# Kernel tuning notes

Hardware: AMD Instinct MI355X
Metric: run time of the kernel (lower is better)

Reference implementation:

```python
import jax, jax.numpy as jnp
import numpy as np

N = 100000      # nodes per graph batch side
E = 1600000     # edges per side
G = 256         # graphs per batch (global_mean_pool segments)
F_IN = 16       # num_node_features


def setup_inputs() -> dict:
    key = jax.random.key(0)
    ks = jax.random.split(key, 14)
    inp = {
        "x1": jax.random.normal(ks[0], (N, F_IN), jnp.float32),
        "edge_index1": jax.random.randint(ks[1], (2, E), 0, N, jnp.int32),
        "batch1": jnp.sort(jax.random.randint(ks[2], (N,), 0, G, jnp.int32)),
        "x2": jax.random.normal(ks[3], (N, F_IN), jnp.float32),
        "edge_index2": jax.random.randint(ks[4], (2, E), 0, N, jnp.int32),
        "batch2": jnp.sort(jax.random.randint(ks[5], (N,), 0, G, jnp.int32)),
        "W1": jax.random.normal(ks[6], (F_IN, 64), jnp.float32) / np.sqrt(F_IN),
        "b1": jnp.zeros((64,), jnp.float32),
        "W2": jax.random.normal(ks[7], (64, 64), jnp.float32) / np.sqrt(64.0),
        "b2": jnp.zeros((64,), jnp.float32),
        "Wf1": jax.random.normal(ks[8], (128, 64), jnp.float32) / np.sqrt(128.0),
        "bf1": jnp.zeros((64,), jnp.float32),
        "Wf2": jax.random.normal(ks[9], (64, 2), jnp.float32) / np.sqrt(64.0),
        "bf2": jnp.zeros((2,), jnp.float32),
    }
    return inp


def _gcn_conv(x, W, b, src, dst):
    """PyG GCNConv: out = D^{-1/2}(A+I)D^{-1/2} (x W) + b, with self-loops."""
    n = x.shape[0]
    sl = jnp.arange(n, dtype=src.dtype)
    s = jnp.concatenate([src, sl])  # [E+N]
    d = jnp.concatenate([dst, sl])
    deg = jax.ops.segment_sum(jnp.ones_like(s, x.dtype), d, num_segments=n)
    dinv = jax.lax.rsqrt(deg)  # deg >= 1 due to self-loops
    h = x @ W                  # transform before scatter (fewer bytes moved when out_dim small)
    norm = (dinv[s] * dinv[d])[:, None]
    msg = h[s] * norm          # [E+N, 64] gather
    return jax.ops.segment_sum(msg, d, num_segments=n) + b


def _global_mean_pool(x, batch):
    s = jax.ops.segment_sum(x, batch, num_segments=G)
    c = jax.ops.segment_sum(jnp.ones((x.shape[0],), x.dtype), batch, num_segments=G)
    return s / jnp.maximum(c, 1.0)[:, None]


def _embed_graph(x, edge_index, batch, W1, b1, W2, b2):
    src, dst = edge_index[0], edge_index[1]
    h = jax.nn.relu(_gcn_conv(x, W1, b1, src, dst))
    h = jax.nn.relu(_gcn_conv(h, W2, b2, src, dst))
    return _global_mean_pool(h, batch)  # [G, 64]


def reference(x1, edge_index1, batch1, x2, edge_index2, batch2,
              W1, b1, W2, b2, Wf1, bf1, Wf2, bf2):
    emb1 = _embed_graph(x1, edge_index1, batch1, W1, b1, W2, b2)
    emb2 = _embed_graph(x2, edge_index2, batch2, W1, b1, W2, b2)
    combined = jnp.concatenate([emb1, emb2], axis=1)  # [G, 128]
    out = jax.nn.relu(combined @ Wf1 + bf1)
    return out @ Wf2 + bf2  # [G, 2]
```

## Files before the change

### kernel.cpp

```cpp
#include <hip/hip_runtime.h>
#include <hip/hip_fp16.h>

#define F_IN 16
#define F_HID 64
#define NPG 8
#define NPG16 4
#define SCAN_CHUNK 1024
#define EPB 4096
#define BKN 1024


__device__ inline void load_edge4(const int* __restrict__ ei1, const int* __restrict__ ei2,
                                  int E, int n, int e4, int4& s4, int4& d4) {
    if (e4 < E) {
        s4 = *(const int4*)(ei1 + e4);
        d4 = *(const int4*)(ei1 + E + e4);
    } else {
        int eb = e4 - E;
        s4 = *(const int4*)(ei2 + eb);
        d4 = *(const int4*)(ei2 + E + eb);
        s4.x += n; s4.y += n; s4.z += n; s4.w += n;
        d4.x += n; d4.y += n; d4.z += n; d4.w += n;
    }
}


__global__ void histA_kernel(const int* __restrict__ ei1, const int* __restrict__ ei2,
                             int E, int n, unsigned* __restrict__ count,
                             int nblkA, int NBK, int E2) {
    __shared__ unsigned hist[256];
    for (int i = threadIdx.x; i < NBK; i += 256) hist[i] = 0;
    __syncthreads();
    int base = blockIdx.x * EPB;
    #pragma unroll
    for (int r = 0; r < EPB / 1024; ++r) {
        int e4 = base + r * 1024 + threadIdx.x * 4;
        if (e4 + 4 <= E2) {
            int4 s4, d4;
            load_edge4(ei1, ei2, E, n, e4, s4, d4);
            atomicAdd(&hist[d4.x >> 10], 1u);
            atomicAdd(&hist[d4.y >> 10], 1u);
            atomicAdd(&hist[d4.z >> 10], 1u);
            atomicAdd(&hist[d4.w >> 10], 1u);
        } else if (e4 < E2) {
            for (int e = e4; e < E2; ++e) {
                int d = (e < E) ? ei1[E + e] : (ei2[e] + n);
                atomicAdd(&hist[d >> 10], 1u);
            }
        }
    }
    __syncthreads();
    for (int i = threadIdx.x; i < NBK; i += 256)
        count[(size_t)i * nblkA + blockIdx.x] = hist[i];
}

__global__ void scan1_kernel(const unsigned* __restrict__ a, unsigned* __restrict__ bsum, int N) {
    __shared__ unsigned s[256];
    int base = blockIdx.x * SCAN_CHUNK;
    unsigned t = 0;
    for (int i = threadIdx.x; i < SCAN_CHUNK; i += 256) {
        int idx = base + i;
        if (idx < N) t += a[idx];
    }
    s[threadIdx.x] = t;
    __syncthreads();
    for (int o = 128; o > 0; o >>= 1) {
        if (threadIdx.x < o) s[threadIdx.x] += s[threadIdx.x + o];
        __syncthreads();
    }
    if (threadIdx.x == 0) bsum[blockIdx.x] = s[0];
}

__global__ void scan2_kernel(unsigned* __restrict__ bsum, int nb) {
    if (threadIdx.x == 0 && blockIdx.x == 0) {
        unsigned run = 0;
        for (int i = 0; i < nb; ++i) { unsigned v = bsum[i]; bsum[i] = run; run += v; }
    }
}

__global__ void scan3g_kernel(unsigned* __restrict__ a, const unsigned* __restrict__ bsum, int N) {
    __shared__ unsigned s[256];
    int tid = threadIdx.x;
    int base = blockIdx.x * SCAN_CHUNK;
    unsigned loc[4];
    unsigned t = 0;
    #pragma unroll
    for (int j = 0; j < 4; ++j) {
        int idx = base + tid * 4 + j;
        loc[j] = (idx < N) ? a[idx] : 0u;
        t += loc[j];
    }
    s[tid] = t;
    __syncthreads();
    for (int o = 1; o < 256; o <<= 1) {
        unsigned v = (tid >= o) ? s[tid - o] : 0u;
        __syncthreads();
        s[tid] += v;
        __syncthreads();
    }
    unsigned off = bsum[blockIdx.x] + s[tid] - t;
    #pragma unroll
    for (int j = 0; j < 4; ++j) {
        int idx = base + tid * 4 + j;
        if (idx < N) a[idx] = off;
        off += loc[j];
    }
}

__global__ void passA2_kernel(const int* __restrict__ ei1, const int* __restrict__ ei2,
                              int E, int n, const unsigned* __restrict__ cbase,
                              unsigned* __restrict__ pairs, int nblkA, int NBK, int E2) {
    __shared__ unsigned cur[256];
    for (int i = threadIdx.x; i < NBK; i += 256)
        cur[i] = cbase[(size_t)i * nblkA + blockIdx.x];
    __syncthreads();
    int base = blockIdx.x * EPB;
    #pragma unroll
    for (int r = 0; r < EPB / 1024; ++r) {
        int e4 = base + r * 1024 + threadIdx.x * 4;
        if (e4 + 4 <= E2) {
            int4 s4, d4;
            load_edge4(ei1, ei2, E, n, e4, s4, d4);
            unsigned p;
            p = atomicAdd(&cur[d4.x >> 10], 1u);
            pairs[p] = ((unsigned)(d4.x & 1023) << 18) | (unsigned)s4.x;
            p = atomicAdd(&cur[d4.y >> 10], 1u);
            pairs[p] = ((unsigned)(d4.y & 1023) << 18) | (unsigned)s4.y;
            p = atomicAdd(&cur[d4.z >> 10], 1u);
            pairs[p] = ((unsigned)(d4.z & 1023) << 18) | (unsigned)s4.z;
            p = atomicAdd(&cur[d4.w >> 10], 1u);
            pairs[p] = ((unsigned)(d4.w & 1023) << 18) | (unsigned)s4.w;
        } else if (e4 < E2) {
            for (int e = e4; e < E2; ++e) {
                int s = (e < E) ? ei1[e] : (ei2[e - E] + n);
                int d = (e < E) ? ei1[E + e] : (ei2[e] + n);
                unsigned p = atomicAdd(&cur[d >> 10], 1u);
                pairs[p] = ((unsigned)(d & 1023) << 18) | (unsigned)s;
            }
        }
    }
}

__global__ void bucketB_kernel(const unsigned* __restrict__ pairs,
                               const unsigned* __restrict__ cbase,
                               const float* __restrict__ x1, const float* __restrict__ x2,
                               int* __restrict__ row_start, float* __restrict__ dinv,
                               __half* __restrict__ xs, int* __restrict__ csr_src,
                               int n, int n2, int E2, int nblkA, int NBK) {
    __shared__ unsigned cnt[BKN];
    __shared__ int cur[BKN];
    __shared__ unsigned s[256];
    int b = blockIdx.x;
    int nodebase = b * BKN;
    int nn = n2 - nodebase; if (nn > BKN) nn = BKN;
    unsigned begin = cbase[(size_t)b * nblkA];
    unsigned end = (b + 1 < NBK) ? cbase[(size_t)(b + 1) * nblkA] : (unsigned)E2;
    int t = threadIdx.x;

    for (int i = t; i < BKN; i += 256) cnt[i] = 0;
    __syncthreads();
    for (unsigned i = begin + t; i < end; i += 256)
        atomicAdd(&cnt[pairs[i] >> 18], 1u);
    __syncthreads();

    unsigned loc[4];
    unsigned tot = 0;
    #pragma unroll
    for (int j = 0; j < 4; ++j) { loc[j] = cnt[t * 4 + j]; tot += loc[j]; }
    s[t] = tot;
    __syncthreads();
    for (int o = 1; o < 256; o <<= 1) {
        unsigned v = (t >= o) ? s[t - o] : 0u;
        __syncthreads();
        s[t] += v;
        __syncthreads();
    }
    unsigned off = begin + s[t] - tot;
    #pragma unroll
    for (int j = 0; j < 4; ++j) {
        int i = t * 4 + j;
        if (i < nn) {
            int node = nodebase + i;
            row_start[node] = (int)off;
            cur[i] = (int)off;
            float di = rsqrtf((float)loc[j] + 1.0f);
            dinv[node] = di;
            const float* xr = (node < n) ? (x1 + (size_t)node * F_IN)
                                         : (x2 + (size_t)(node - n) * F_IN);
            const float4* xin = (const float4*)xr;
            union { float4 f4; __half2 h2[4]; } u;
            __half2* xo = (__half2*)(xs + (size_t)node * F_IN);
            #pragma unroll
            for (int c = 0; c < 2; ++c) {
                float4 v0 = xin[2 * c], v1 = xin[2 * c + 1];
                u.h2[0] = __float22half2_rn(make_float2(v0.x * di, v0.y * di));
                u.h2[1] = __float22half2_rn(make_float2(v0.z * di, v0.w * di));
                u.h2[2] = __float22half2_rn(make_float2(v1.x * di, v1.y * di));
                u.h2[3] = __float22half2_rn(make_float2(v1.z * di, v1.w * di));
                *(float4*)(xo + 4 * c) = u.f4;
            }
        }
        off += loc[j];
    }
    __syncthreads();
    for (unsigned i = begin + t; i < end; i += 256) {
        unsigned v = pairs[i];
        int pos = atomicAdd(&cur[v >> 18], 1);
        csr_src[pos] = (int)(v & 0x3FFFFu);
    }
    if (b == 0 && t == 0) row_start[n2] = E2;
}


__device__ inline void acc_row2(float4& a, float2 r) {
    union { float2 f2; __half2 h2[2]; } u; u.f2 = r;
    float2 lo = __half22float2(u.h2[0]), hi = __half22float2(u.h2[1]);
    a.x += lo.x; a.y += lo.y; a.z += hi.x; a.w += hi.y;
}

__global__ void agg16_kernel(const int* __restrict__ csr_src, const int* __restrict__ row_start,
                             const __half* __restrict__ xs, const float* __restrict__ dinv,
                             __half* __restrict__ xagg, int n2) {
    int g4 = threadIdx.x >> 2, lane4 = threadIdx.x & 3;
    int gid = blockIdx.x * 64 + g4;
    int base = gid * NPG16;
    if (base >= n2) return;
    int end_n = base + NPG16;
    if (end_n > n2) end_n = n2;
    for (int node = base; node < end_n; ++node) {
        int start = row_start[node], end = row_start[node + 1];
        float4 acc = make_float4(0.f, 0.f, 0.f, 0.f);
        int e = start;
        for (; e + 4 <= end; e += 4) {
            int i0 = csr_src[e + 0], i1 = csr_src[e + 1];
            int i2 = csr_src[e + 2], i3 = csr_src[e + 3];
            float2 r0 = *(const float2*)(xs + (size_t)i0 * F_IN + lane4 * 4);
            float2 r1 = *(const float2*)(xs + (size_t)i1 * F_IN + lane4 * 4);
            float2 r2 = *(const float2*)(xs + (size_t)i2 * F_IN + lane4 * 4);
            float2 r3 = *(const float2*)(xs + (size_t)i3 * F_IN + lane4 * 4);
            acc_row2(acc, r0); acc_row2(acc, r1); acc_row2(acc, r2); acc_row2(acc, r3);
        }
        for (; e < end; ++e) {
            float2 r0 = *(const float2*)(xs + (size_t)csr_src[e] * F_IN + lane4 * 4);
            acc_row2(acc, r0);
        }
        float2 rs = *(const float2*)(xs + (size_t)node * F_IN + lane4 * 4);
        acc_row2(acc, rs);
        float di = dinv[node];
        union { float2 f2; __half2 h2[2]; } u;
        u.h2[0] = __float22half2_rn(make_float2(acc.x * di, acc.y * di));
        u.h2[1] = __float22half2_rn(make_float2(acc.z * di, acc.w * di));
        *(float2*)(xagg + (size_t)node * F_IN + lane4 * 4) = u.f2;
    }
}

__global__ __launch_bounds__(256) void mlp_kernel(
        const __half* __restrict__ xagg, const float* __restrict__ dinv,
        const float* __restrict__ W1, const float* __restrict__ b1,
        const float* __restrict__ W2, __half* __restrict__ hw, int n2) {
    __shared__ __align__(16) float w1[F_IN * F_HID];
    __shared__ __align__(16) float w2[F_HID * F_HID];
    __shared__ float b1s[F_HID];
    __shared__ __align__(16) float xl[64][20];
    __shared__ __align__(16) float h1s[64][68];
    int t = threadIdx.x;
    for (int i = t; i < F_IN * F_HID; i += 256) w1[i] = W1[i];
    for (int i = t; i < F_HID * F_HID; i += 256) w2[i] = W2[i];
    if (t < F_HID) b1s[t] = b1[t];

    int base = blockIdx.x * 64;
    int m = t >> 2, jg = t & 3, j0 = jg * 16;
    int node = base + m;
    bool valid = node < n2;

    {
        int k0 = jg * 4;
        if (valid) {
            union { float2 f2; __half2 h2[2]; } u;
            u.f2 = *(const float2*)(xagg + (size_t)node * F_IN + k0);
            float2 lo = __half22float2(u.h2[0]), hi = __half22float2(u.h2[1]);
            *(float4*)&xl[m][k0] = make_float4(lo.x, lo.y, hi.x, hi.y);
        }
    }
    __syncthreads();

    float acc[16];
    #pragma unroll
    for (int jj = 0; jj < 16; ++jj) acc[jj] = 0.0f;
    if (valid) {
        #pragma unroll
        for (int k = 0; k < F_IN; ++k) {
            float xv = xl[m][k];
            const float4* wp = (const float4*)(w1 + k * F_HID + j0);
            #pragma unroll
            for (int q = 0; q < 4; ++q) {
                float4 wv = wp[q];
                acc[4 * q + 0] += xv * wv.x;
                acc[4 * q + 1] += xv * wv.y;
                acc[4 * q + 2] += xv * wv.z;
                acc[4 * q + 3] += xv * wv.w;
            }
        }
        float di = dinv[node];
        #pragma unroll
        for (int jj = 0; jj < 16; ++jj)
            h1s[m][j0 + jj] = fmaxf(acc[jj] + b1s[j0 + jj], 0.0f) * di;
    }
    __syncthreads();

    float o[16];
    #pragma unroll
    for (int jj = 0; jj < 16; ++jj) o[jj] = 0.0f;
    if (valid) {
        #pragma unroll 8
        for (int k = 0; k < F_HID; ++k) {
            float hv = h1s[m][k];
            const float4* wp = (const float4*)(w2 + k * F_HID + j0);
            #pragma unroll
            for (int q = 0; q < 4; ++q) {
                float4 wv = wp[q];
                o[4 * q + 0] += hv * wv.x;
                o[4 * q + 1] += hv * wv.y;
                o[4 * q + 2] += hv * wv.z;
                o[4 * q + 3] += hv * wv.w;
            }
        }
        union { float4 f4; __half2 h2[4]; } p0, p1;
        #pragma unroll
        for (int q = 0; q < 4; ++q) {
            p0.h2[q] = __float22half2_rn(make_float2(o[2 * q], o[2 * q + 1]));
            p1.h2[q] = __float22half2_rn(make_float2(o[8 + 2 * q], o[8 + 2 * q + 1]));
        }
        float4* dst = (float4*)(hw + (size_t)node * F_HID + j0);
        dst[0] = p0.f4;
        dst[1] = p1.f4;
    }
}

__global__ void aggpool_kernel(const int* __restrict__ csr_src, const int* __restrict__ row_start,
                               const __half* __restrict__ hw, const float* __restrict__ dinv,
                               const int* __restrict__ batch1, const int* __restrict__ batch2,
                               const float* __restrict__ b2,
                               float* __restrict__ pooled, float* __restrict__ cnt,
                               int n, int G) {
    int n2 = 2 * n;
    int g16 = threadIdx.x >> 4, lane16 = threadIdx.x & 15;
    int gid = blockIdx.x * 16 + g16;
    int base = gid * NPG;
    if (base >= n2) return;
    int end_n = base + NPG;
    if (end_n > n2) end_n = n2;

    const float4 bias = *(const float4*)(b2 + lane16 * 4);
    float4 pacc = make_float4(0.f, 0.f, 0.f, 0.f);
    float count = 0.0f;
    int cur_b = (base < n) ? batch1[base] : (batch2[base - n] + G);

    for (int node = base; node < end_n; ++node) {
        int b = (node < n) ? batch1[node] : (batch2[node - n] + G);
        if (b != cur_b) {
            atomicAdd(&pooled[cur_b * F_HID + lane16 * 4 + 0], pacc.x);
            atomicAdd(&pooled[cur_b * F_HID + lane16 * 4 + 1], pacc.y);
            atomicAdd(&pooled[cur_b * F_HID + lane16 * 4 + 2], pacc.z);
            atomicAdd(&pooled[cur_b * F_HID + lane16 * 4 + 3], pacc.w);
            if (lane16 == 0) atomicAdd(&cnt[cur_b], count);
            pacc = make_float4(0.f, 0.f, 0.f, 0.f); count = 0.0f; cur_b = b;
        }
        int start = row_start[node], end = row_start[node + 1];
        float4 acc = make_float4(0.f, 0.f, 0.f, 0.f);
        int e = start;
        for (; e + 8 <= end; e += 8) {
            int i0 = csr_src[e + 0], i1 = csr_src[e + 1];
            int i2 = csr_src[e + 2], i3 = csr_src[e + 3];
            int i4 = csr_src[e + 4], i5 = csr_src[e + 5];
            int i6 = csr_src[e + 6], i7 = csr_src[e + 7];
            float2 r0 = *(const float2*)(hw + (size_t)i0 * F_HID + lane16 * 4);
            float2 r1 = *(const float2*)(hw + (size_t)i1 * F_HID + lane16 * 4);
            float2 r2 = *(const float2*)(hw + (size_t)i2 * F_HID + lane16 * 4);
            float2 r3 = *(const float2*)(hw + (size_t)i3 * F_HID + lane16 * 4);
            float2 r4 = *(const float2*)(hw + (size_t)i4 * F_HID + lane16 * 4);
            float2 r5 = *(const float2*)(hw + (size_t)i5 * F_HID + lane16 * 4);
            float2 r6 = *(const float2*)(hw + (size_t)i6 * F_HID + lane16 * 4);
            float2 r7 = *(const float2*)(hw + (size_t)i7 * F_HID + lane16 * 4);
            acc_row2(acc, r0); acc_row2(acc, r1); acc_row2(acc, r2); acc_row2(acc, r3);
            acc_row2(acc, r4); acc_row2(acc, r5); acc_row2(acc, r6); acc_row2(acc, r7);
        }
        for (; e < end; ++e) {
            float2 r0 = *(const float2*)(hw + (size_t)csr_src[e] * F_HID + lane16 * 4);
            acc_row2(acc, r0);
        }
        float2 rs = *(const float2*)(hw + (size_t)node * F_HID + lane16 * 4);
        acc_row2(acc, rs);
        float di = dinv[node];
        pacc.x += fmaxf(bias.x + di * acc.x, 0.0f);
        pacc.y += fmaxf(bias.y + di * acc.y, 0.0f);
        pacc.z += fmaxf(bias.z + di * acc.z, 0.0f);
        pacc.w += fmaxf(bias.w + di * acc.w, 0.0f);
        count += 1.0f;
    }
    atomicAdd(&pooled[cur_b * F_HID + lane16 * 4 + 0], pacc.x);
    atomicAdd(&pooled[cur_b * F_HID + lane16 * 4 + 1], pacc.y);
    atomicAdd(&pooled[cur_b * F_HID + lane16 * 4 + 2], pacc.z);
    atomicAdd(&pooled[cur_b * F_HID + lane16 * 4 + 3], pacc.w);
    if (lane16 == 0) atomicAdd(&cnt[cur_b], count);
}

__global__ void head_kernel(const float* __restrict__ p1, const float* __restrict__ c1,
                            const float* __restrict__ p2, const float* __restrict__ c2,
                            const float* __restrict__ Wf1, const float* __restrict__ bf1,
                            const float* __restrict__ Wf2, const float* __restrict__ bf2,
                            float* __restrict__ out) {
    int g = blockIdx.x;
    int j = threadIdx.x;
    __shared__ float comb[128];
    float inv1 = 1.0f / fmaxf(c1[g], 1.0f);
    float inv2 = 1.0f / fmaxf(c2[g], 1.0f);
    comb[j] = p1[g * 64 + j] * inv1;
    comb[64 + j] = p2[g * 64 + j] * inv2;
    __syncthreads();
    float acc = bf1[j];
    #pragma unroll
    for (int k = 0; k < 128; ++k) acc += comb[k] * Wf1[k * 64 + j];
    float h = fmaxf(acc, 0.0f);
    float o0 = h * Wf2[j * 2 + 0];
    float o1 = h * Wf2[j * 2 + 1];
    #pragma unroll
    for (int off = 32; off > 0; off >>= 1) {
        o0 += __shfl_down(o0, off);
        o1 += __shfl_down(o1, off);
    }
    if (j == 0) {
        out[g * 2 + 0] = o0 + bf2[0];
        out[g * 2 + 1] = o1 + bf2[1];
    }
}

extern "C" void kernel_launch(void* const* d_in, const int* in_sizes, int n_in,
                              void* d_out, int out_size, void* d_ws, size_t ws_size,
                              hipStream_t stream) {
    const float* x1     = (const float*)d_in[0];
    const int*   ei1    = (const int*)d_in[1];
    const int*   batch1 = (const int*)d_in[2];
    const float* x2     = (const float*)d_in[3];
    const int*   ei2    = (const int*)d_in[4];
    const int*   batch2 = (const int*)d_in[5];
    const float* W1     = (const float*)d_in[6];
    const float* b1     = (const float*)d_in[7];
    const float* W2     = (const float*)d_in[8];
    const float* b2     = (const float*)d_in[9];
    const float* Wf1    = (const float*)d_in[10];
    const float* bf1    = (const float*)d_in[11];
    const float* Wf2    = (const float*)d_in[12];
    const float* bf2    = (const float*)d_in[13];
    float* out = (float*)d_out;

    const int n = in_sizes[0] / F_IN;
    const int E = in_sizes[1] / 2;
    const int G = out_size / 2;
    const int n2 = 2 * n;
    const int E2 = 2 * E;
    const int NBK = (n2 + BKN - 1) / BKN;
    const int nblkA = (E2 + EPB - 1) / EPB;
    const int N_A = NBK * nblkA;
    const int nbA = (N_A + SCAN_CHUNK - 1) / SCAN_CHUNK;

    char* ws = (char*)d_ws;
    size_t off = 0;
    unsigned* count  = (unsigned*)(ws + off); off += (((size_t)N_A + 63) & ~63ull) * 4;
    unsigned* bsumA  = (unsigned*)(ws + off); off += (size_t)((nbA + 63) & ~63) * 4;
    int* row_start   = (int*)(ws + off);      off += (((size_t)n2 + 64) & ~63ull) * 4;
    int* csr_src     = (int*)(ws + off);      off += (size_t)E2 * 4;
    float* dinv      = (float*)(ws + off);    off += (size_t)n2 * 4;
    __half* xs       = (__half*)(ws + off);   off += (size_t)n2 * F_IN * 2;
    __half* xagg     = (__half*)(ws + off);   off += (size_t)n2 * F_IN * 2;
    __half* hwbuf    = (__half*)(ws + off);   off += (size_t)n2 * F_HID * 2;
    float* pooled    = (float*)(ws + off);    off += 2 * (size_t)G * F_HID * 4;
    float* cnt       = (float*)(ws + off);    off += 2 * (size_t)G * 4;

    unsigned* pairs = (unsigned*)hwbuf;

    hipMemsetAsync(pooled, 0, (2 * (size_t)G * F_HID + 2 * (size_t)G) * sizeof(float), stream);

    histA_kernel<<<nblkA, 256, 0, stream>>>(ei1, ei2, E, n, count, nblkA, NBK, E2);
    scan1_kernel<<<nbA, 256, 0, stream>>>(count, bsumA, N_A);
    scan2_kernel<<<1, 64, 0, stream>>>(bsumA, nbA);
    scan3g_kernel<<<nbA, 256, 0, stream>>>(count, bsumA, N_A);
    passA2_kernel<<<nblkA, 256, 0, stream>>>(ei1, ei2, E, n, count, pairs, nblkA, NBK, E2);
    bucketB_kernel<<<NBK, 256, 0, stream>>>(pairs, count, x1, x2, row_start, dinv, xs,
                                            csr_src, n, n2, E2, nblkA, NBK);

    const int groups16 = (n2 + NPG16 - 1) / NPG16;
    agg16_kernel<<<(groups16 + 63) / 64, 256, 0, stream>>>(csr_src, row_start, xs, dinv, xagg, n2);

    mlp_kernel<<<(n2 + 63) / 64, 256, 0, stream>>>(xagg, dinv, W1, b1, W2, hwbuf, n2);

    const int groups = (n2 + NPG - 1) / NPG;
    aggpool_kernel<<<(groups + 15) / 16, 256, 0, stream>>>(
        csr_src, row_start, hwbuf, dinv, batch1, batch2, b2, pooled, cnt, n, G);

    head_kernel<<<G, 64, 0, stream>>>(pooled, cnt, pooled + (size_t)G * F_HID, cnt + G,
                                      Wf1, bf1, Wf2, bf2, out);
}
```

Baseline: 327.5 us.

## Fuse first-layer aggregation into MLP kernel and widen aggpool gather loads

Removes the separate agg16 kernel: the first-layer neighbour aggregation is now done inside the MLP kernel, with the aggregated features written straight into shared memory instead of being round-tripped through a half-precision xagg buffer. This drops a launch and the xagg write and read, and keeps the aggregated features in fp32 rather than rounding them to half. Separately, aggpool now uses 8 lanes per node with 16-byte loads (8 halves) instead of 16 lanes with 8-byte loads, and handles 4 nodes per group instead of 8. That gives more groups but fewer lanes each, and each thread issues twice as many atomics per flush.

```diff
diff --git a/kernel.cpp b/kernel.cpp
--- a/kernel.cpp
+++ b/kernel.cpp
@@ -3,8 +3,7 @@
 
 #define F_IN 16
 #define F_HID 64
-#define NPG 8
-#define NPG16 4
+#define NPG 4
 #define SCAN_CHUNK 1024
 #define EPB 4096
 #define BKN 1024
@@ -218,44 +217,17 @@
     a.x += lo.x; a.y += lo.y; a.z += hi.x; a.w += hi.y;
 }
 
-__global__ void agg16_kernel(const int* __restrict__ csr_src, const int* __restrict__ row_start,
-                             const __half* __restrict__ xs, const float* __restrict__ dinv,
-                             __half* __restrict__ xagg, int n2) {
-    int g4 = threadIdx.x >> 2, lane4 = threadIdx.x & 3;
-    int gid = blockIdx.x * 64 + g4;
-    int base = gid * NPG16;
-    if (base >= n2) return;
-    int end_n = base + NPG16;
-    if (end_n > n2) end_n = n2;
-    for (int node = base; node < end_n; ++node) {
-        int start = row_start[node], end = row_start[node + 1];
-        float4 acc = make_float4(0.f, 0.f, 0.f, 0.f);
-        int e = start;
-        for (; e + 4 <= end; e += 4) {
-            int i0 = csr_src[e + 0], i1 = csr_src[e + 1];
-            int i2 = csr_src[e + 2], i3 = csr_src[e + 3];
-            float2 r0 = *(const float2*)(xs + (size_t)i0 * F_IN + lane4 * 4);
-            float2 r1 = *(const float2*)(xs + (size_t)i1 * F_IN + lane4 * 4);
-            float2 r2 = *(const float2*)(xs + (size_t)i2 * F_IN + lane4 * 4);
-            float2 r3 = *(const float2*)(xs + (size_t)i3 * F_IN + lane4 * 4);
-            acc_row2(acc, r0); acc_row2(acc, r1); acc_row2(acc, r2); acc_row2(acc, r3);
-        }
-        for (; e < end; ++e) {
-            float2 r0 = *(const float2*)(xs + (size_t)csr_src[e] * F_IN + lane4 * 4);
-            acc_row2(acc, r0);
-        }
-        float2 rs = *(const float2*)(xs + (size_t)node * F_IN + lane4 * 4);
-        acc_row2(acc, rs);
-        float di = dinv[node];
-        union { float2 f2; __half2 h2[2]; } u;
-        u.h2[0] = __float22half2_rn(make_float2(acc.x * di, acc.y * di));
-        u.h2[1] = __float22half2_rn(make_float2(acc.z * di, acc.w * di));
-        *(float2*)(xagg + (size_t)node * F_IN + lane4 * 4) = u.f2;
-    }
-}
-
-__global__ __launch_bounds__(256) void mlp_kernel(
-        const __half* __restrict__ xagg, const float* __restrict__ dinv,
+__device__ inline void acc_row4(float4& a0, float4& a1, float4 r) {
+    union { float4 f4; __half2 h2[4]; } u; u.f4 = r;
+    float2 p0 = __half22float2(u.h2[0]), p1 = __half22float2(u.h2[1]);
+    float2 p2 = __half22float2(u.h2[2]), p3 = __half22float2(u.h2[3]);
+    a0.x += p0.x; a0.y += p0.y; a0.z += p1.x; a0.w += p1.y;
+    a1.x += p2.x; a1.y += p2.y; a1.z += p3.x; a1.w += p3.y;
+}
+
+__global__ __launch_bounds__(256) void aggmlp_kernel(
+        const int* __restrict__ csr_src, const int* __restrict__ row_start,
+        const __half* __restrict__ xs, const float* __restrict__ dinv,
         const float* __restrict__ W1, const float* __restrict__ b1,
         const float* __restrict__ W2, __half* __restrict__ hw, int n2) {
     __shared__ __align__(16) float w1[F_IN * F_HID];
@@ -272,15 +244,30 @@
     int m = t >> 2, jg = t & 3, j0 = jg * 16;
     int node = base + m;
     bool valid = node < n2;
-
-    {
-        int k0 = jg * 4;
-        if (valid) {
-            union { float2 f2; __half2 h2[2]; } u;
-            u.f2 = *(const float2*)(xagg + (size_t)node * F_IN + k0);
-            float2 lo = __half22float2(u.h2[0]), hi = __half22float2(u.h2[1]);
-            *(float4*)&xl[m][k0] = make_float4(lo.x, lo.y, hi.x, hi.y);
-        }
+    float di = 0.0f;
+
+    if (valid) {
+        int start = row_start[node], end = row_start[node + 1];
+        float4 acc = make_float4(0.f, 0.f, 0.f, 0.f);
+        int e = start;
+        for (; e + 4 <= end; e += 4) {
+            int i0 = csr_src[e + 0], i1 = csr_src[e + 1];
+            int i2 = csr_src[e + 2], i3 = csr_src[e + 3];
+            float2 r0 = *(const float2*)(xs + (size_t)i0 * F_IN + jg * 4);
+            float2 r1 = *(const float2*)(xs + (size_t)i1 * F_IN + jg * 4);
+            float2 r2 = *(const float2*)(xs + (size_t)i2 * F_IN + jg * 4);
+            float2 r3 = *(const float2*)(xs + (size_t)i3 * F_IN + jg * 4);
+            acc_row2(acc, r0); acc_row2(acc, r1); acc_row2(acc, r2); acc_row2(acc, r3);
+        }
+        for (; e < end; ++e) {
+            float2 r0 = *(const float2*)(xs + (size_t)csr_src[e] * F_IN + jg * 4);
+            acc_row2(acc, r0);
+        }
+        float2 rs = *(const float2*)(xs + (size_t)node * F_IN + jg * 4);
+        acc_row2(acc, rs);
+        di = dinv[node];
+        *(float4*)&xl[m][jg * 4] =
+            make_float4(acc.x * di, acc.y * di, acc.z * di, acc.w * di);
     }
     __syncthreads();
 
@@ -301,7 +288,6 @@
                 acc[4 * q + 3] += xv * wv.w;
             }
         }
-        float di = dinv[node];
         #pragma unroll
         for (int jj = 0; jj < 16; ++jj)
             h1s[m][j0 + jj] = fmaxf(acc[jj] + b1s[j0 + jj], 0.0f) * di;
@@ -344,65 +330,70 @@
                                float* __restrict__ pooled, float* __restrict__ cnt,
                                int n, int G) {
     int n2 = 2 * n;
-    int g16 = threadIdx.x >> 4, lane16 = threadIdx.x & 15;
-    int gid = blockIdx.x * 16 + g16;
+    int g8 = threadIdx.x >> 3, lane8 = threadIdx.x & 7;
+    int gid = blockIdx.x * 32 + g8;
     int base = gid * NPG;
     if (base >= n2) return;
     int end_n = base + NPG;
     if (end_n > n2) end_n = n2;
 
-    const float4 bias = *(const float4*)(b2 + lane16 * 4);
-    float4 pacc = make_float4(0.f, 0.f, 0.f, 0.f);
+    const float4 bias0 = *(const float4*)(b2 + lane8 * 8);
+    const float4 bias1 = *(const float4*)(b2 + lane8 * 8 + 4);
+    float4 pacc0 = make_float4(0.f, 0.f, 0.f, 0.f);
+    float4 pacc1 = make_float4(0.f, 0.f, 0.f, 0.f);
     float count = 0.0f;
     int cur_b = (base < n) ? batch1[base] : (batch2[base - n] + G);
 
     for (int node = base; node < end_n; ++node) {
         int b = (node < n) ? batch1[node] : (batch2[node - n] + G);
         if (b != cur_b) {
-            atomicAdd(&pooled[cur_b * F_HID + lane16 * 4 + 0], pacc.x);
-            atomicAdd(&pooled[cur_b * F_HID + lane16 * 4 + 1], pacc.y);
-            atomicAdd(&pooled[cur_b * F_HID + lane16 * 4 + 2], pacc.z);
-            atomicAdd(&pooled[cur_b * F_HID + lane16 * 4 + 3], pacc.w);
-            if (lane16 == 0) atomicAdd(&cnt[cur_b], count);
-            pacc = make_float4(0.f, 0.f, 0.f, 0.f); count = 0.0f; cur_b = b;
+            float* pp = pooled + (size_t)cur_b * F_HID + lane8 * 8;
+            atomicAdd(pp + 0, pacc0.x); atomicAdd(pp + 1, pacc0.y);
+            atomicAdd(pp + 2, pacc0.z); atomicAdd(pp + 3, pacc0.w);
+            atomicAdd(pp + 4, pacc1.x); atomicAdd(pp + 5, pacc1.y);
+            atomicAdd(pp + 6, pacc1.z); atomicAdd(pp + 7, pacc1.w);
+            if (lane8 == 0) atomicAdd(&cnt[cur_b], count);
+            pacc0 = make_float4(0.f, 0.f, 0.f, 0.f);
+            pacc1 = make_float4(0.f, 0.f, 0.f, 0.f);
+            count = 0.0f; cur_b = b;
         }
         int start = row_start[node], end = row_start[node + 1];
-        float4 acc = make_float4(0.f, 0.f, 0.f, 0.f);
+        float4 a0 = make_float4(0.f, 0.f, 0.f, 0.f);
+        float4 a1 = make_float4(0.f, 0.f, 0.f, 0.f);
         int e = start;
-        for (; e + 8 <= end; e += 8) {
+        for (; e + 4 <= end; e += 4) {
             int i0 = csr_src[e + 0], i1 = csr_src[e + 1];
             int i2 = csr_src[e + 2], i3 = csr_src[e + 3];
-            int i4 = csr_src[e + 4], i5 = csr_src[e + 5];
-            int i6 = csr_src[e + 6], i7 = csr_src[e + 7];
-            float2 r0 = *(const float2*)(hw + (size_t)i0 * F_HID + lane16 * 4);
-            float2 r1 = *(const float2*)(hw + (size_t)i1 * F_HID + lane16 * 4);
-            float2 r2 = *(const float2*)(hw + (size_t)i2 * F_HID + lane16 * 4);
-            float2 r3 = *(const float2*)(hw + (size_t)i3 * F_HID + lane16 * 4);
-            float2 r4 = *(const float2*)(hw + (size_t)i4 * F_HID + lane16 * 4);
-            float2 r5 = *(const float2*)(hw + (size_t)i5 * F_HID + lane16 * 4);
-            float2 r6 = *(const float2*)(hw + (size_t)i6 * F_HID + lane16 * 4);
-            float2 r7 = *(const float2*)(hw + (size_t)i7 * F_HID + lane16 * 4);
-            acc_row2(acc, r0); acc_row2(acc, r1); acc_row2(acc, r2); acc_row2(acc, r3);
-            acc_row2(acc, r4); acc_row2(acc, r5); acc_row2(acc, r6); acc_row2(acc, r7);
+            float4 r0 = *(const float4*)(hw + (size_t)i0 * F_HID + lane8 * 8);
+            float4 r1 = *(const float4*)(hw + (size_t)i1 * F_HID + lane8 * 8);
+            float4 r2 = *(const float4*)(hw + (size_t)i2 * F_HID + lane8 * 8);
+            float4 r3 = *(const float4*)(hw + (size_t)i3 * F_HID + lane8 * 8);
+            acc_row4(a0, a1, r0); acc_row4(a0, a1, r1);
+            acc_row4(a0, a1, r2); acc_row4(a0, a1, r3);
         }
         for (; e < end; ++e) {
-            float2 r0 = *(const float2*)(hw + (size_t)csr_src[e] * F_HID + lane16 * 4);
-            acc_row2(acc, r0);
-        }
-        float2 rs = *(const float2*)(hw + (size_t)node * F_HID + lane16 * 4);
-        acc_row2(acc, rs);
+            float4 r0 = *(const float4*)(hw + (size_t)csr_src[e] * F_HID + lane8 * 8);
+            acc_row4(a0, a1, r0);
+        }
+        float4 rs = *(const float4*)(hw + (size_t)node * F_HID + lane8 * 8);
+        acc_row4(a0, a1, rs);
         float di = dinv[node];
-        pacc.x += fmaxf(bias.x + di * acc.x, 0.0f);
-        pacc.y += fmaxf(bias.y + di * acc.y, 0.0f);
-        pacc.z += fmaxf(bias.z + di * acc.z, 0.0f);
-        pacc.w += fmaxf(bias.w + di * acc.w, 0.0f);
+        pacc0.x += fmaxf(bias0.x + di * a0.x, 0.0f);
+        pacc0.y += fmaxf(bias0.y + di * a0.y, 0.0f);
+        pacc0.z += fmaxf(bias0.z + di * a0.z, 0.0f);
+        pacc0.w += fmaxf(bias0.w + di * a0.w, 0.0f);
+        pacc1.x += fmaxf(bias1.x + di * a1.x, 0.0f);
+        pacc1.y += fmaxf(bias1.y + di * a1.y, 0.0f);
+        pacc1.z += fmaxf(bias1.z + di * a1.z, 0.0f);
+        pacc1.w += fmaxf(bias1.w + di * a1.w, 0.0f);
         count += 1.0f;
     }
-    atomicAdd(&pooled[cur_b * F_HID + lane16 * 4 + 0], pacc.x);
-    atomicAdd(&pooled[cur_b * F_HID + lane16 * 4 + 1], pacc.y);
-    atomicAdd(&pooled[cur_b * F_HID + lane16 * 4 + 2], pacc.z);
-    atomicAdd(&pooled[cur_b * F_HID + lane16 * 4 + 3], pacc.w);
-    if (lane16 == 0) atomicAdd(&cnt[cur_b], count);
+    float* pp = pooled + (size_t)cur_b * F_HID + lane8 * 8;
+    atomicAdd(pp + 0, pacc0.x); atomicAdd(pp + 1, pacc0.y);
+    atomicAdd(pp + 2, pacc0.z); atomicAdd(pp + 3, pacc0.w);
+    atomicAdd(pp + 4, pacc1.x); atomicAdd(pp + 5, pacc1.y);
+    atomicAdd(pp + 6, pacc1.z); atomicAdd(pp + 7, pacc1.w);
+    if (lane8 == 0) atomicAdd(&cnt[cur_b], count);
 }
 
 __global__ void head_kernel(const float* __restrict__ p1, const float* __restrict__ c1,
@@ -472,7 +463,6 @@
     int* csr_src     = (int*)(ws + off);      off += (size_t)E2 * 4;
     float* dinv      = (float*)(ws + off);    off += (size_t)n2 * 4;
     __half* xs       = (__half*)(ws + off);   off += (size_t)n2 * F_IN * 2;
-    __half* xagg     = (__half*)(ws + off);   off += (size_t)n2 * F_IN * 2;
     __half* hwbuf    = (__half*)(ws + off);   off += (size_t)n2 * F_HID * 2;
     float* pooled    = (float*)(ws + off);    off += 2 * (size_t)G * F_HID * 4;
     float* cnt       = (float*)(ws + off);    off += 2 * (size_t)G * 4;
@@ -489,13 +479,11 @@
     bucketB_kernel<<<NBK, 256, 0, stream>>>(pairs, count, x1, x2, row_start, dinv, xs,
                                             csr_src, n, n2, E2, nblkA, NBK);
 
-    const int groups16 = (n2 + NPG16 - 1) / NPG16;
-    agg16_kernel<<<(groups16 + 63) / 64, 256, 0, stream>>>(csr_src, row_start, xs, dinv, xagg, n2);
-
-    mlp_kernel<<<(n2 + 63) / 64, 256, 0, stream>>>(xagg, dinv, W1, b1, W2, hwbuf, n2);
+    aggmlp_kernel<<<(n2 + 63) / 64, 256, 0, stream>>>(csr_src, row_start, xs, dinv,
+                                                      W1, b1, W2, hwbuf, n2);
 
     const int groups = (n2 + NPG - 1) / NPG;
-    aggpool_kernel<<<(groups + 15) / 16, 256, 0, stream>>>(
+    aggpool_kernel<<<(groups + 31) / 32, 256, 0, stream>>>(
         csr_src, row_start, hwbuf, dinv, batch1, batch2, b2, pooled, cnt, n, G);
 
     head_kernel<<<G, 64, 0, stream>>>(pooled, cnt, pooled + (size_t)G * F_HID, cnt + G,
```

Result: slower. 435.5 us (+33.0%).
